# Kernel optimization log

Hardware: AMD Instinct MI355X
Metric: run time of the kernel (lower is better)

Reference implementation:

```python
import jax, jax.numpy as jnp
import numpy as np
import math

SEQ = 16384      # total ragged tokens
DIM = 1280       # vision hidden size
HEADS = 16
HDIM = DIM // HEADS  # 80
NSEG = 16        # number of segments (images); equal lengths of 1024


def rotate_half(x):
    x1, x2 = jnp.split(x, 2, axis=-1)
    return jnp.concatenate([-x2, x1], axis=-1)


def setup_inputs() -> dict:
    key = jax.random.key(0)
    ks = jax.random.split(key, 6)
    hidden_states = jax.random.normal(ks[0], (SEQ, DIM), dtype=jnp.float32)
    # rotary tables over the full head_dim (Qwen vision style: freqs duplicated)
    inv_freq = 1.0 / (10000.0 ** (jnp.arange(0, HDIM, 2, dtype=jnp.float32) / HDIM))
    pos = jnp.arange(SEQ, dtype=jnp.float32)
    freqs = jnp.outer(pos, inv_freq)                      # [S, HDIM/2]
    emb = jnp.concatenate([freqs, freqs], axis=-1)        # [S, HDIM]
    cos, sin = jnp.cos(emb), jnp.sin(emb)
    w_qkv = jax.random.normal(ks[1], (3 * DIM, DIM), dtype=jnp.float32) * 0.02
    b_qkv = jax.random.normal(ks[2], (3 * DIM,), dtype=jnp.float32) * 0.02
    w_proj = jax.random.normal(ks[3], (DIM, DIM), dtype=jnp.float32) * 0.02
    b_proj = jax.random.normal(ks[4], (DIM,), dtype=jnp.float32) * 0.02
    cu_seqlens = jnp.arange(NSEG + 1, dtype=jnp.int32) * (SEQ // NSEG)
    return {"hidden_states": hidden_states, "cos": cos, "sin": sin,
            "w_qkv": w_qkv, "b_qkv": b_qkv, "w_proj": w_proj, "b_proj": b_proj,
            "cu_seqlens": cu_seqlens}


def reference(hidden_states, cos, sin, w_qkv, b_qkv, w_proj, b_proj, cu_seqlens):
    S, D = hidden_states.shape
    hd = cos.shape[-1]
    nh = D // hd
    nseg = cu_seqlens.shape[0] - 1
    L = S // nseg  # equal segment lengths (matches cu_seqlens built in setup)

    qkv = hidden_states @ w_qkv.T + b_qkv                 # [S, 3D]
    qkv = qkv.reshape(S, 3, nh, hd)
    q, k, v = qkv[:, 0], qkv[:, 1], qkv[:, 2]             # [S, H, hd]

    # rotary (computed in float32, as in the original)
    c = cos[:, None, :]
    s = sin[:, None, :]
    q = q * c + rotate_half(q) * s
    k = k * c + rotate_half(k) * s

    # block-diagonal attention: reshape ragged-equal segments into a batch dim
    qs = q.reshape(nseg, L, nh, hd)
    ks = k.reshape(nseg, L, nh, hd)
    vs = v.reshape(nseg, L, nh, hd)

    scale = 1.0 / math.sqrt(hd)
    scores = jnp.einsum('bqhd,bkhd->bhqk', qs, ks) * scale   # [nseg, H, L, L]
    probs = jax.nn.softmax(scores, axis=-1)
    out = jnp.einsum('bhqk,bkhd->bqhd', probs, vs)           # [nseg, L, H, hd]
    out = out.reshape(S, D)
    return out @ w_proj.T + b_proj
```

## Files before the change

### kernel.cpp

```cpp
#include <hip/hip_runtime.h>

#define SEQ 16384
#define DIM 1280
#define NH 16
#define HD 80
#define NSEG 16
#define SEGL 1024

typedef __attribute__((ext_vector_type(8))) short bf16x8;
typedef __attribute__((ext_vector_type(4))) float f32x4;

__device__ inline unsigned short f2bf(float f){
  unsigned int x = __builtin_bit_cast(unsigned int, f);
  unsigned int r = (x + 0x7FFFu + ((x >> 16) & 1u)) >> 16;
  return (unsigned short)r;
}
__device__ inline float bf2f(unsigned short u){
  unsigned int x = ((unsigned int)u) << 16;
  return __builtin_bit_cast(float, x);
}
__device__ inline int cvtpk_bf16(float lo, float hi){
  int r;
  asm("v_cvt_pk_bf16_f32 %0, %1, %2" : "=v"(r) : "v"(lo), "v"(hi));
  return r;
}

__device__ inline void gload16(const unsigned short* g, unsigned short* l){
  __builtin_amdgcn_global_load_lds((const __attribute__((address_space(1))) void*)g,
                                   (__attribute__((address_space(3))) void*)l, 16, 0, 0);
}

__global__ __launch_bounds__(256) void pack_bf16_kernel(const float* __restrict__ src,
                                                        unsigned short* __restrict__ dst, int n4){
  int i = blockIdx.x * 256 + threadIdx.x;
  if (i >= n4) return;
  float4 v = ((const float4*)src)[i];
  ushort4 o;
  o.x = f2bf(v.x); o.y = f2bf(v.y); o.z = f2bf(v.z); o.w = f2bf(v.w);
  ((ushort4*)dst)[i] = o;
}

template<int EPI>
__global__ __launch_bounds__(512, 2) void gemm256_kernel(const unsigned short* __restrict__ A,
    const unsigned short* __restrict__ B, const float* __restrict__ bias,
    void* __restrict__ Cout, int M, int N, int K){
  __shared__ __attribute__((aligned(16))) unsigned short As[2][16384];
  __shared__ __attribute__((aligned(16))) unsigned short Bs[2][16384];
  const int nwg = gridDim.x;
  int bid = blockIdx.x;
  int swz = (bid & 7) * (nwg >> 3) + (bid >> 3);
  const int ntn = N >> 8;
  const int tm = (swz / ntn) << 8;
  const int tn = (swz % ntn) << 8;
  const int tid = threadIdx.x;
  const int wid = tid >> 6, l = tid & 63;
  const int lr = l & 15, lh = l >> 4;
  const int wrM = (wid >> 2) << 7;
  const int wcN = (wid & 3) << 6;
  const int NITER = K >> 7;

  const int srow = wid*8 + (l >> 3);
  const int scol = ((l & 7) ^ (l >> 3)) << 3;
  const int sldsu = wid << 9;

  const unsigned short* Ag = A + (size_t)tm * K;
  const unsigned short* Bg = B + (size_t)tn * K;

  const int ck0 = (lh*8) ^ ((l & 7) << 3);
  const int ck1 = (32 + lh*8) ^ ((l & 7) << 3);
  const int raA = (wrM + lr) << 6;
  const int raB = (wcN + lr) << 6;

  f32x4 zf = {0.f,0.f,0.f,0.f};
  f32x4 acc[8][4];
  #pragma unroll
  for (int i=0;i<8;i++)
    #pragma unroll
    for (int j=0;j<4;j++) acc[i][j] = zf;

#define STAGE_A(tile, h, q) gload16(Ag + (size_t)((h)*128 + (q)*64 + srow)*K + ((tile)<<6) + scol, \
                                    &As[(tile)&1][(h)*8192 + (q)*4096 + sldsu])
#define STAGE_B(tile, h, q) gload16(Bg + (size_t)((h)*128 + (q)*64 + srow)*K + ((tile)<<6) + scol, \
                                    &Bs[(tile)&1][(h)*8192 + (q)*4096 + sldsu])
#define RD_A(b, MOFF) \
  _Pragma("unroll") \
  for (int mi=0; mi<4; ++mi){ \
    a[0][mi] = *(const bf16x8*)&As[b][raA + ((MOFF)+mi)*1024 + ck0]; \
    a[1][mi] = *(const bf16x8*)&As[b][raA + ((MOFF)+mi)*1024 + ck1]; }
#define RD_B(b, NOFF, BREG) \
  _Pragma("unroll") \
  for (int nj=0; nj<2; ++nj){ \
    BREG[0][nj] = *(const bf16x8*)&Bs[b][raB + ((NOFF)+nj)*1024 + ck0]; \
    BREG[1][nj] = *(const bf16x8*)&Bs[b][raB + ((NOFF)+nj)*1024 + ck1]; }
#define BAR() __builtin_amdgcn_s_barrier();
#define QMFMA(MB, NB, BREG) \
  __builtin_amdgcn_s_setprio(1); \
  _Pragma("unroll") \
  for (int mi=0; mi<4; ++mi){ \
    _Pragma("unroll") \
    for (int nj=0; nj<2; ++nj){ \
      acc[(MB)+mi][(NB)+nj] = __builtin_amdgcn_mfma_f32_16x16x32_bf16(a[0][mi], BREG[0][nj], acc[(MB)+mi][(NB)+nj], 0,0,0); \
      acc[(MB)+mi][(NB)+nj] = __builtin_amdgcn_mfma_f32_16x16x32_bf16(a[1][mi], BREG[1][nj], acc[(MB)+mi][(NB)+nj], 0,0,0); \
    } \
  } \
  __builtin_amdgcn_s_setprio(0); \
  __builtin_amdgcn_s_barrier();

  #pragma unroll
  for (int q=0;q<2;q++){ STAGE_A(0,0,q); }
  #pragma unroll
  for (int q=0;q<2;q++){ STAGE_A(0,1,q); }
  #pragma unroll
  for (int q=0;q<2;q++){ STAGE_B(0,0,q); }
  #pragma unroll
  for (int q=0;q<2;q++){ STAGE_B(0,1,q); }
  #pragma unroll
  for (int q=0;q<2;q++){ STAGE_B(1,0,q); }
  #pragma unroll
  for (int q=0;q<2;q++){ STAGE_B(1,1,q); }
  #pragma unroll
  for (int q=0;q<2;q++){ STAGE_A(1,0,q); }
  #pragma unroll
  for (int q=0;q<2;q++){ STAGE_A(1,1,q); }
  asm volatile("s_waitcnt vmcnt(8)" ::: "memory");
  __builtin_amdgcn_s_barrier();

  for (int i=0; i<NITER; ++i){
    const int T = 2*i;
    const bool st = (i+1 < NITER);
    bf16x8 a[2][4], bx[2][2], by[2][2];

    RD_B(0, 0, bx); RD_A(0, 0);
    BAR(); QMFMA(0, 0, bx);

    RD_B(0, 2, by);
    BAR(); QMFMA(0, 2, by);

    RD_A(0, 4);
    if (st){ STAGE_B(T+2, 0, 0); STAGE_B(T+2, 0, 1); }
    BAR(); QMFMA(4, 2, by);

    if (st){
      STAGE_B(T+2, 1, 0); STAGE_B(T+2, 1, 1);
      STAGE_A(T+2, 0, 0); STAGE_A(T+2, 0, 1);
      asm volatile("s_waitcnt vmcnt(6)" ::: "memory");
    } else {
      asm volatile("s_waitcnt vmcnt(0)" ::: "memory");
    }
    BAR(); QMFMA(4, 0, bx);

    RD_B(1, 0, bx); RD_A(1, 0);
    if (st){ STAGE_A(T+2, 1, 0); STAGE_A(T+2, 1, 1); }
    BAR(); QMFMA(0, 0, bx);

    RD_B(1, 2, by);
    BAR(); QMFMA(0, 2, by);

    RD_A(1, 4);
    if (st){ STAGE_B(T+3, 0, 0); STAGE_B(T+3, 0, 1); STAGE_B(T+3, 1, 0); STAGE_B(T+3, 1, 1); }
    BAR(); QMFMA(4, 2, by);

    if (st){
      STAGE_A(T+3, 0, 0); STAGE_A(T+3, 0, 1); STAGE_A(T+3, 1, 0); STAGE_A(T+3, 1, 1);
      asm volatile("s_waitcnt vmcnt(8)" ::: "memory");
    }
    BAR(); QMFMA(4, 0, bx);
  }

#undef STAGE_A
#undef STAGE_B
#undef RD_A
#undef RD_B
#undef BAR
#undef QMFMA

  #pragma unroll
  for (int nj=0;nj<4;nj++){
    int col = tn + wcN + nj*16 + lr;
    float bv = bias[col];
    if (EPI == 0){
      unsigned short* Q = (unsigned short*)Cout;
      int which = col / DIM;
      int rem = col - which*DIM;
      int hh = rem / HD;
      int d = rem - hh*HD;
      size_t base = (size_t)(which*NH + hh) * SEQ;
      #pragma unroll
      for (int mi=0;mi<8;mi++){
        #pragma unroll
        for (int r=0;r<4;r++){
          int row = tm + wrM + mi*16 + lh*4 + r;
          Q[(base + row)*HD + d] = f2bf(acc[mi][nj][r] + bv);
        }
      }
    } else {
      float* C = (float*)Cout;
      #pragma unroll
      for (int mi=0;mi<8;mi++){
        #pragma unroll
        for (int r=0;r<4;r++){
          int row = tm + wrM + mi*16 + lh*4 + r;
          C[(size_t)row*N + col] = acc[mi][nj][r] + bv;
        }
      }
    }
  }
}

__global__ __launch_bounds__(256) void rope_kernel(unsigned short* __restrict__ QKV,
    const float* __restrict__ cosb, const float* __restrict__ sinb){
  unsigned int gid = blockIdx.x * 256 + threadIdx.x;
  int pd = gid % 40;
  unsigned int row = gid / 40;
  int s = row % SEQ;
  float f = (row < (unsigned)(NH*SEQ)) ? (0.111803398874989485f * 1.4426950408889634f) : 1.0f;
  unsigned short* p = QKV + (size_t)row * HD;
  float c  = cosb[s*HD + pd];
  float sn = sinb[s*HD + pd];
  float x1 = bf2f(p[pd]);
  float x2 = bf2f(p[pd+40]);
  p[pd]    = f2bf((x1*c - x2*sn)*f);
  p[pd+40] = f2bf((x2*c + x1*sn)*f);
}

__global__ __launch_bounds__(256) void transpose_v_kernel(const unsigned short* __restrict__ V,
                                                          unsigned short* __restrict__ Vt){
  __shared__ unsigned short L[64*84];
  int bid = blockIdx.x;
  int h  = bid >> 8;
  int st = bid & 255;
  int s0 = st * 64;
  int tid = threadIdx.x;
  const unsigned short* Vs = V + (size_t)h * SEQ * HD;
  #pragma unroll
  for (int i=0;i<3;i++){
    int u = i*256 + tid;
    if (u < 640){
      int r = u / 10, c = u % 10;
      uint4 v = *(const uint4*)(Vs + (size_t)(s0 + r)*HD + c*8);
      unsigned int* p = (unsigned int*)&L[r*84 + c*8];
      p[0] = v.x; p[1] = v.y; p[2] = v.z; p[3] = v.w;
    }
  }
  __syncthreads();
  unsigned short* Vd = Vt + (size_t)h * HD * SEQ;
  #pragma unroll
  for (int i=0;i<5;i++){
    int u = i*256 + tid;
    int d = u >> 4, g = u & 15;
    int sb = g*4;
    int pg = ((g>>3)<<3) + ((g&3)<<1) + ((g>>2)&1);
    unsigned int w0 = (unsigned int)L[(sb+0)*84 + d] | ((unsigned int)L[(sb+1)*84 + d] << 16);
    unsigned int w1 = (unsigned int)L[(sb+2)*84 + d] | ((unsigned int)L[(sb+3)*84 + d] << 16);
    uint2 o = {w0, w1};
    *(uint2*)(Vd + (size_t)d*SEQ + s0 + pg*4) = o;
  }
}

__global__ __launch_bounds__(512) void attn_kernel(const unsigned short* __restrict__ QKV,
                                                   const unsigned short* __restrict__ Vt,
                                                   unsigned short* __restrict__ AO){
  int bid = blockIdx.x;
  int qt  = bid & 7;
  int h   = (bid >> 3) & 15;
  int seg = bid >> 7;
  int tid = threadIdx.x, wid = tid >> 6, l = tid & 63;
  int lr = l & 15, lh = l >> 4;
  const unsigned short* Qb = QKV + (size_t)(0*NH + h) * SEQ * HD;
  const unsigned short* Kb = QKV + (size_t)(1*NH + h) * SEQ * HD;
  const unsigned short* Vtb = Vt + (size_t)h * HD * SEQ;
  int q0 = seg*SEGL + qt*128;
  __shared__ __attribute__((aligned(16))) unsigned short Ksm[5152];
  __shared__ __attribute__((aligned(16))) unsigned short Vtsm[5120];
  bf16x8 qf[3];
  {
    const unsigned short* qp = Qb + (size_t)(q0 + wid*16 + lr) * HD;
    #pragma unroll
    for (int c=0;c<3;c++){
      int d0 = c*32 + lh*8;
      bf16x8 z = {0,0,0,0,0,0,0,0};
      qf[c] = (d0 < HD) ? *(const bf16x8*)(qp + d0) : z;
    }
  }
  f32x4 zf = {0.f,0.f,0.f,0.f};
  f32x4 o[5];
  #pragma unroll
  for (int dt=0;dt<5;dt++) o[dt] = zf;
  float m = -1e30f, lsum = 0.f;
  for (int kt=0; kt<16; kt++){
    int k0 = seg*SEGL + kt*64;
    const unsigned short* Ksrc = Kb + (size_t)k0 * HD;
    gload16(Ksrc + (wid*64 + l)*8, &Ksm[wid*512]);
    if (wid < 2){
      gload16(Ksrc + (512 + wid*64 + l)*8, &Ksm[4096 + wid*512]);
    } else {
      int uv = (wid-2)*64 + l;
      int d = uv >> 3, c16 = uv & 7;
      gload16(Vtb + (size_t)d*SEQ + k0 + ((c16 ^ (d & 7)) << 3), &Vtsm[(wid-2)*512]);
    }
    if (wid < 4){
      int uv = 384 + wid*64 + l;
      int d = uv >> 3, c16 = uv & 7;
      gload16(Vtb + (size_t)d*SEQ + k0 + ((c16 ^ (d & 7)) << 3), &Vtsm[3072 + wid*512]);
    }
    __syncthreads();
    f32x4 s[4];
    #pragma unroll
    for (int n=0;n<4;n++) s[n] = zf;
    #pragma unroll
    for (int c=0;c<3;c++){
      #pragma unroll
      for (int n=0;n<4;n++){
        bf16x8 kf = *(const bf16x8*)&Ksm[(n*16+lr)*80 + c*32 + lh*8];
        s[n] = __builtin_amdgcn_mfma_f32_16x16x32_bf16(kf, qf[c], s[n], 0,0,0);
      }
    }
    float pm = s[0][0];
    #pragma unroll
    for (int n=0;n<4;n++)
      #pragma unroll
      for (int r=0;r<4;r++) pm = fmaxf(pm, s[n][r]);
    pm = fmaxf(pm, __shfl_xor(pm, 16));
    pm = fmaxf(pm, __shfl_xor(pm, 32));
    if (!__all(pm <= m + 8.f)){
      float mn = fmaxf(m, pm);
      float corr = exp2f(m - mn);
      lsum *= corr;
      #pragma unroll
      for (int dt=0;dt<5;dt++)
        #pragma unroll
        for (int r=0;r<4;r++) o[dt][r] *= corr;
      m = mn;
    }
    float rs = 0.f;
    #pragma unroll
    for (int n=0;n<4;n++)
      #pragma unroll
      for (int r=0;r<4;r++){
        float p = exp2f(s[n][r] - m);
        s[n][r] = p;
        rs += p;
      }
    rs += __shfl_xor(rs, 16);
    rs += __shfl_xor(rs, 32);
    lsum += rs;
    int w[8];
    #pragma unroll
    for (int n=0;n<4;n++){
      w[2*n]   = cvtpk_bf16(s[n][0], s[n][1]);
      w[2*n+1] = cvtpk_bf16(s[n][2], s[n][3]);
    }
    #pragma unroll
    for (int kc=0;kc<2;kc++){
      union { bf16x8 v; int u[4]; } pf;
      pf.u[0] = w[4*kc+0]; pf.u[1] = w[4*kc+1];
      pf.u[2] = w[4*kc+2]; pf.u[3] = w[4*kc+3];
      #pragma unroll
      for (int dt=0;dt<5;dt++){
        int row = dt*16 + lr;
        bf16x8 vf = *(const bf16x8*)&Vtsm[row*64 + ((kc*32 + lh*8) ^ ((lr & 7) << 3))];
        o[dt] = __builtin_amdgcn_mfma_f32_16x16x32_bf16(vf, pf.v, o[dt], 0,0,0);
      }
    }
    __syncthreads();
  }
  float inv = 1.0f / lsum;
  int qrow = q0 + wid*16 + lr;
  unsigned short* op = AO + (size_t)qrow*DIM + h*HD;
  #pragma unroll
  for (int dt=0;dt<5;dt++){
    unsigned int w0 = (unsigned int)cvtpk_bf16(o[dt][0]*inv, o[dt][1]*inv);
    unsigned int w1 = (unsigned int)cvtpk_bf16(o[dt][2]*inv, o[dt][3]*inv);
    uint2 ov = {w0, w1};
    *(uint2*)(op + dt*16 + lh*4) = ov;
  }
}

extern "C" void kernel_launch(void* const* d_in, const int* in_sizes, int n_in,
                              void* d_out, int out_size, void* d_ws, size_t ws_size,
                              hipStream_t stream){
  const float* hs    = (const float*)d_in[0];
  const float* cosb  = (const float*)d_in[1];
  const float* sinb  = (const float*)d_in[2];
  const float* wqkv  = (const float*)d_in[3];
  const float* bqkv  = (const float*)d_in[4];
  const float* wproj = (const float*)d_in[5];
  const float* bproj = (const float*)d_in[6];
  float* out = (float*)d_out;

  unsigned short* Abf    = (unsigned short*)d_ws;
  unsigned short* Wqkvb  = Abf + (size_t)SEQ*DIM;
  unsigned short* Wprojb = Wqkvb + (size_t)3*DIM*DIM;
  unsigned short* QKVb   = Wprojb + (size_t)DIM*DIM;
  unsigned short* Vtb    = QKVb + (size_t)3*SEQ*DIM;
  unsigned short* AObf   = Abf;

  pack_bf16_kernel<<<(SEQ*DIM/4)/256, 256, 0, stream>>>(hs, Abf, SEQ*DIM/4);
  pack_bf16_kernel<<<(3*DIM*DIM/4)/256, 256, 0, stream>>>(wqkv, Wqkvb, 3*DIM*DIM/4);
  pack_bf16_kernel<<<(DIM*DIM/4)/256, 256, 0, stream>>>(wproj, Wprojb, DIM*DIM/4);

  gemm256_kernel<0><<<(SEQ/256)*((3*DIM)/256), 512, 0, stream>>>(Abf, Wqkvb, bqkv,
                                                                 (void*)QKVb, SEQ, 3*DIM, DIM);

  rope_kernel<<<(2*NH*SEQ*40)/256, 256, 0, stream>>>(QKVb, cosb, sinb);

  transpose_v_kernel<<<NH*(SEQ/64), 256, 0, stream>>>(QKVb + (size_t)2*NH*SEQ*HD, Vtb);

  attn_kernel<<<NSEG*NH*(SEGL/128), 512, 0, stream>>>(QKVb, Vtb, AObf);

  gemm256_kernel<1><<<(SEQ/256)*(DIM/256), 512, 0, stream>>>(AObf, Wprojb, bproj,
                                                             (void*)out, SEQ, DIM, DIM);
}
```

Baseline: 496.0 us.

## Write V transposed from QKV GEMM epilogue and remap attention block order

The QKV GEMM epilogue now writes the V third straight into the transposed, permuted Vt layout that attention consumes, using packed bf16 conversion and 8-byte stores. This removes the separate transpose kernel and its read and write of the V buffer. Attention block indices are also remapped so that query tiles of the same head and segment are spread across the grid differently, which may change L2 locality for K and V. The Vt stores stride by SEQ per column, so epilogue write coalescing gets worse.

```diff
diff --git a/kernel.cpp b/kernel.cpp
--- a/kernel.cpp
+++ b/kernel.cpp
@@ -43,7 +43,7 @@
 template<int EPI>
 __global__ __launch_bounds__(512, 2) void gemm256_kernel(const unsigned short* __restrict__ A,
     const unsigned short* __restrict__ B, const float* __restrict__ bias,
-    void* __restrict__ Cout, int M, int N, int K){
+    void* __restrict__ Cout, unsigned short* __restrict__ Vtg, int M, int N, int K){
   __shared__ __attribute__((aligned(16))) unsigned short As[2][16384];
   __shared__ __attribute__((aligned(16))) unsigned short Bs[2][16384];
   const int nwg = gridDim.x;
@@ -179,18 +179,33 @@
     int col = tn + wcN + nj*16 + lr;
     float bv = bias[col];
     if (EPI == 0){
-      unsigned short* Q = (unsigned short*)Cout;
       int which = col / DIM;
       int rem = col - which*DIM;
       int hh = rem / HD;
       int d = rem - hh*HD;
-      size_t base = (size_t)(which*NH + hh) * SEQ;
-      #pragma unroll
-      for (int mi=0;mi<8;mi++){
+      if (which == 2){
+        unsigned short* Vd = Vtg + ((size_t)hh * HD + d) * SEQ;
         #pragma unroll
-        for (int r=0;r<4;r++){
-          int row = tm + wrM + mi*16 + lh*4 + r;
-          Q[(base + row)*HD + d] = f2bf(acc[mi][nj][r] + bv);
+        for (int mi=0;mi<8;mi++){
+          int row0 = tm + wrM + mi*16 + lh*4;
+          int g = (row0 >> 2) & 15;
+          int pg = ((g>>3)<<3) + ((g&3)<<1) + ((g>>2)&1);
+          int s = (row0 & ~63) + pg*4;
+          unsigned int w0 = (unsigned int)cvtpk_bf16(acc[mi][nj][0]+bv, acc[mi][nj][1]+bv);
+          unsigned int w1 = (unsigned int)cvtpk_bf16(acc[mi][nj][2]+bv, acc[mi][nj][3]+bv);
+          uint2 ov = {w0, w1};
+          *(uint2*)(Vd + s) = ov;
+        }
+      } else {
+        unsigned short* Q = (unsigned short*)Cout;
+        size_t base = (size_t)(which*NH + hh) * SEQ;
+        #pragma unroll
+        for (int mi=0;mi<8;mi++){
+          #pragma unroll
+          for (int r=0;r<4;r++){
+            int row = tm + wrM + mi*16 + lh*4 + r;
+            Q[(base + row)*HD + d] = f2bf(acc[mi][nj][r] + bv);
+          }
         }
       }
     } else {
@@ -223,47 +238,14 @@
   p[pd+40] = f2bf((x2*c + x1*sn)*f);
 }
 
-__global__ __launch_bounds__(256) void transpose_v_kernel(const unsigned short* __restrict__ V,
-                                                          unsigned short* __restrict__ Vt){
-  __shared__ unsigned short L[64*84];
-  int bid = blockIdx.x;
-  int h  = bid >> 8;
-  int st = bid & 255;
-  int s0 = st * 64;
-  int tid = threadIdx.x;
-  const unsigned short* Vs = V + (size_t)h * SEQ * HD;
-  #pragma unroll
-  for (int i=0;i<3;i++){
-    int u = i*256 + tid;
-    if (u < 640){
-      int r = u / 10, c = u % 10;
-      uint4 v = *(const uint4*)(Vs + (size_t)(s0 + r)*HD + c*8);
-      unsigned int* p = (unsigned int*)&L[r*84 + c*8];
-      p[0] = v.x; p[1] = v.y; p[2] = v.z; p[3] = v.w;
-    }
-  }
-  __syncthreads();
-  unsigned short* Vd = Vt + (size_t)h * HD * SEQ;
-  #pragma unroll
-  for (int i=0;i<5;i++){
-    int u = i*256 + tid;
-    int d = u >> 4, g = u & 15;
-    int sb = g*4;
-    int pg = ((g>>3)<<3) + ((g&3)<<1) + ((g>>2)&1);
-    unsigned int w0 = (unsigned int)L[(sb+0)*84 + d] | ((unsigned int)L[(sb+1)*84 + d] << 16);
-    unsigned int w1 = (unsigned int)L[(sb+2)*84 + d] | ((unsigned int)L[(sb+3)*84 + d] << 16);
-    uint2 o = {w0, w1};
-    *(uint2*)(Vd + (size_t)d*SEQ + s0 + pg*4) = o;
-  }
-}
-
 __global__ __launch_bounds__(512) void attn_kernel(const unsigned short* __restrict__ QKV,
                                                    const unsigned short* __restrict__ Vt,
                                                    unsigned short* __restrict__ AO){
   int bid = blockIdx.x;
-  int qt  = bid & 7;
-  int h   = (bid >> 3) & 15;
-  int seg = bid >> 7;
+  int qt  = (bid >> 3) & 7;
+  int g   = (bid & 7) * 32 + (bid >> 6);
+  int h   = g & 15;
+  int seg = g >> 4;
   int tid = threadIdx.x, wid = tid >> 6, l = tid & 63;
   int lr = l & 15, lh = l >> 4;
   const unsigned short* Qb = QKV + (size_t)(0*NH + h) * SEQ * HD;
@@ -400,14 +382,12 @@
   pack_bf16_kernel<<<(DIM*DIM/4)/256, 256, 0, stream>>>(wproj, Wprojb, DIM*DIM/4);
 
   gemm256_kernel<0><<<(SEQ/256)*((3*DIM)/256), 512, 0, stream>>>(Abf, Wqkvb, bqkv,
-                                                                 (void*)QKVb, SEQ, 3*DIM, DIM);
+                                                                 (void*)QKVb, Vtb, SEQ, 3*DIM, DIM);
 
   rope_kernel<<<(2*NH*SEQ*40)/256, 256, 0, stream>>>(QKVb, cosb, sinb);
 
-  transpose_v_kernel<<<NH*(SEQ/64), 256, 0, stream>>>(QKVb + (size_t)2*NH*SEQ*HD, Vtb);
-
   attn_kernel<<<NSEG*NH*(SEGL/128), 512, 0, stream>>>(QKVb, Vtb, AObf);
 
   gemm256_kernel<1><<<(SEQ/256)*(DIM/256), 512, 0, stream>>>(AObf, Wprojb, bproj,
-                                                             (void*)out, SEQ, DIM, DIM);
-}
+                                                             (void*)out, nullptr, SEQ, DIM, DIM);
+}
```

Result: faster. 467.0 us (-5.8%).
